# Kernel tuning notes

Hardware: AMD Instinct MI355X
Metric: run time of the kernel (lower is better)

The kernel has to match this reference:

```python
import jax, jax.numpy as jnp
import numpy as np

LAMBDA_K_TAU = 0.1
RIDGE = 0.1


def _masked_cov(x, mask, counts):
    """Covariance of masked rows. x: [B,S,D], mask: [B,S] float, counts: [B] float.
    Equivalent to packing the masked rows (batch_2d_tensor) then _torch_cov."""
    xm = x * mask[..., None]
    mean = xm.sum(axis=1) / counts[:, None]                 # [B,D]
    xc = (xm - mean[:, None, :]) * mask[..., None]          # [B,S,D]
    cov = jnp.einsum('bsi,bsj->bij', xc, xc)
    return cov / (counts - 1.0)[:, None, None]


def _calc_label_cov_inv(task_cov, label_cov):
    d = task_cov.shape[-1]
    eye = jnp.eye(d, dtype=task_cov.dtype)
    return jnp.linalg.inv(LAMBDA_K_TAU * label_cov + (1.0 - LAMBDA_K_TAU) * task_cov + RIDGE * eye)


def setup_inputs() -> dict:
    key = jax.random.key(0)
    ks = jax.random.split(key, 6)
    B, S, Q, D = 256, 512, 256, 512
    support_set = jax.random.normal(ks[0], (B, S, D), dtype=jnp.float32)
    support_labels = jax.random.randint(ks[1], (B, S), 0, 2, dtype=jnp.int32)
    query_set = jax.random.normal(ks[2], (B, Q, D), dtype=jnp.float32)
    # lengths in [len//2, len] so both classes are present and counts > 1
    support_set_lengths = jax.random.randint(ks[3], (B,), S // 2, S + 1, dtype=jnp.int32)
    query_set_lengths = jax.random.randint(ks[4], (B,), Q // 2, Q + 1, dtype=jnp.int32)
    log_prediction_scaling = jnp.asarray(np.log(10.0), dtype=jnp.float32)
    return {
        'support_set': support_set,
        'support_labels': support_labels,
        'query_set': query_set,
        'support_set_lengths': support_set_lengths,
        'query_set_lengths': query_set_lengths,
        'log_prediction_scaling': log_prediction_scaling,
    }


def reference(support_set, support_labels, query_set, support_set_lengths,
              query_set_lengths, log_prediction_scaling):
    B, S, D = support_set.shape
    Q = query_set.shape[1]
    f32 = support_set.dtype

    sup_valid = (jnp.arange(S)[None, :] < support_set_lengths[:, None]).astype(f32)  # [B,S]
    mask_pos = (support_labels == 1).astype(f32) * sup_valid                          # [B,S]
    mask_neg = (support_labels == 0).astype(f32) * sup_valid

    pos_counts = mask_pos.sum(axis=1)   # [B]
    neg_counts = mask_neg.sum(axis=1)
    sup_counts = support_set_lengths.astype(f32)

    positive_mean = jnp.einsum('bsd,bs->bd', support_set, mask_pos) / pos_counts[:, None]
    negative_mean = jnp.einsum('bsd,bs->bd', support_set, mask_neg) / neg_counts[:, None]

    cov_mats = _masked_cov(support_set, sup_valid, sup_counts)   # task covariance
    pos_mats = _masked_cov(support_set, mask_pos, pos_counts)    # == cov of packed positives
    neg_mats = _masked_cov(support_set, mask_neg, neg_counts)

    pos_inv = _calc_label_cov_inv(cov_mats, pos_mats)  # [B,D,D]
    neg_inv = _calc_label_cov_inv(cov_mats, neg_mats)

    q_valid = (jnp.arange(Q)[None, :] < query_set_lengths[:, None]).astype(f32)  # [B,Q]

    pos_diff = positive_mean[:, None, :] - query_set  # [B,Q,D]
    neg_diff = negative_mean[:, None, :] - query_set
    pos_maha = jnp.einsum('bik,bkx,bix->bi', pos_diff, pos_inv, pos_diff) * q_valid
    neg_maha = jnp.einsum('bik,bkx,bix->bi', neg_diff, neg_inv, neg_diff) * q_valid

    logit_scale = jnp.exp(log_prediction_scaling)
    # scale is applied inside batch_calculate_mahalanobis_logits AND again in forward
    logits = jnp.stack([neg_maha, pos_maha], axis=-1) * (-1.0) * logit_scale
    return logits * logit_scale  # [B,Q,2]
```

## Files before the change

kernel.cpp:

```cpp
#include <hip/hip_runtime.h>
#include <hip/hip_bf16.h>

#define TPB 256
constexpr int B_ = 256, S_ = 512, D_ = 512, Q_ = 256, NM_ = 512;
constexpr int NB = 64, NT = 8;

typedef _Float16 f16x8 __attribute__((ext_vector_type(8)));
typedef float f32x4 __attribute__((ext_vector_type(4)));

__device__ __forceinline__ void decode_mt(int bid, int W, int& m, int& t){
  int x = bid & 7, r = bid >> 3;
  t = r % W; int u = r / W;
  m = (((u >> 1)*8 + x) << 1) | (u & 1);
}

__device__ __forceinline__ void stage_D(const float* __restrict__ src, size_t ld,
                                        float (*dst)[68], int t)
{
  int r = t >> 2, seg = (t & 3) * 16;
  const float4* s4 = (const float4*)(src + (size_t)r*ld + seg);
  #pragma unroll
  for (int i=0;i<4;i++) *((float4*)&dst[r][seg + i*4]) = s4[i];
}

__device__ __forceinline__ void stage_T(const float* __restrict__ src, size_t ld,
                                        float (*dst)[68], int t)
{
  int r = t >> 2, seg = (t & 3) * 16;
  const float4* s4 = (const float4*)(src + (size_t)r*ld + seg);
  #pragma unroll
  for (int i=0;i<4;i++){
    float4 v = s4[i];
    dst[seg + i*4 + 0][r] = v.x;
    dst[seg + i*4 + 1][r] = v.y;
    dst[seg + i*4 + 2][r] = v.z;
    dst[seg + i*4 + 3][r] = v.w;
  }
}

__global__ __launch_bounds__(TPB) void k_stats(const float* __restrict__ X,
                                               const int* __restrict__ labels,
                                               const int* __restrict__ slen,
                                               float* __restrict__ mu,
                                               float* __restrict__ cnt,
                                               unsigned int* __restrict__ wpbits)
{
  int b = blockIdx.x, t = threadIdx.x;
  __shared__ int lab[S_];
  __shared__ float red[TPB];
  int L = slen[b];
  for (int s = t; s < S_; s += TPB) {
    int lb = labels[b*S_ + s];
    lab[s] = (s < L) ? lb : -1;
  }
  __syncthreads();
  if (t < 16) {
    unsigned int wword = 0;
    for (int i2 = 0; i2 < 32; i2++) if (lab[t*32 + i2] == 1) wword |= (1u << i2);
    wpbits[b*16 + t] = wword;
  }
  int cpi=0, cni=0;
  for (int s=t; s<S_; s+=TPB){ cpi += (lab[s]==1); cni += (lab[s]==0); }
  red[t] = (float)cpi; __syncthreads();
  for (int o=TPB/2;o>0;o>>=1){ if(t<o) red[t]+=red[t+o]; __syncthreads(); }
  float cp = red[0]; __syncthreads();
  red[t] = (float)cni; __syncthreads();
  for (int o=TPB/2;o>0;o>>=1){ if(t<o) red[t]+=red[t+o]; __syncthreads(); }
  float cn = red[0];
  if (t==0){ cnt[b*2+0]=cn; cnt[b*2+1]=cp; }
  float sp0=0,sp1=0,sn0=0,sn1=0;
  const float* Xb = X + (size_t)b*S_*D_;
  for (int s=0;s<S_;s++){
    int e = lab[s];
    if (e < 0) continue;
    float x0 = Xb[(size_t)s*D_ + t];
    float x1 = Xb[(size_t)s*D_ + t + 256];
    if (e==1){ sp0+=x0; sp1+=x1; } else { sn0+=x0; sn1+=x1; }
  }
  float stv = (float)L;
  float* mb = mu + (size_t)b*3*D_;
  mb[0*D_ + t] = sn0/cn;        mb[0*D_ + t+256] = sn1/cn;
  mb[1*D_ + t] = sp0/cp;        mb[1*D_ + t+256] = sp1/cp;
  mb[2*D_ + t] = (sn0+sp0)/stv; mb[2*D_ + t+256] = (sn1+sp1)/stv;
}

__global__ __launch_bounds__(TPB) void k_prep(const float* __restrict__ X,
                                              const int* __restrict__ slen,
                                              unsigned short* __restrict__ Xvh,
                                              unsigned short* __restrict__ Xvl)
{
  int b = blockIdx.y, z = blockIdx.x;
  int d0 = (z>>3)*64, s0 = (z&7)*64;
  int t = threadIdx.x;
  __shared__ float Tl[64][65];
  const float* src = X + ((size_t)b*S_ + s0)*D_ + d0;
  { int r = t>>2, seg = (t&3)*16;
    const float4* s4 = (const float4*)(src + (size_t)r*D_ + seg);
    #pragma unroll
    for (int i=0;i<4;i++){ float4 v = s4[i];
      Tl[seg+i*4+0][r]=v.x; Tl[seg+i*4+1][r]=v.y; Tl[seg+i*4+2][r]=v.z; Tl[seg+i*4+3][r]=v.w; } }
  __syncthreads();
  int L = slen[b];
  int dr = t>>2, sc = (t&3)*16;
  union U16 { unsigned short u[8]; uint4 v; };
  U16 H[2], Lo[2];
  #pragma unroll
  for (int g=0; g<2; g++)
    #pragma unroll
    for (int i=0;i<8;i++){
      int si = sc + g*8 + i;
      float x = (s0+si < L) ? Tl[dr][si] : 0.f;
      _Float16 hh = (_Float16)x;
      float lo = x - (float)hh;
      H[g].u[i]  = __builtin_bit_cast(unsigned short, hh);
      Lo[g].u[i] = __builtin_bit_cast(unsigned short, (_Float16)lo);
    }
  size_t o = ((size_t)b*D_ + d0+dr)*S_ + s0 + sc;
  *(uint4*)(Xvh+o)   = H[0].v;  *(uint4*)(Xvh+o+8) = H[1].v;
  *(uint4*)(Xvl+o)   = Lo[0].v; *(uint4*)(Xvl+o+8) = Lo[1].v;
}

__global__ __launch_bounds__(TPB,2) void k_gram(const unsigned short* __restrict__ Xvh,
                                                const unsigned short* __restrict__ Xvl,
                                                const unsigned int* __restrict__ wpbits,
                                                const float* __restrict__ mu,
                                                const float* __restrict__ cnt,
                                                const int* __restrict__ slen,
                                                float* __restrict__ A)
{
  __shared__ unsigned short sAvh[128][32], sAvl[128][32], sAph[128][32], sApl[128][32],
                            sBvh[128][32], sBvl[128][32];
  int id = blockIdx.x;
  int g = id>>3;
  int b = (g/10)*8 + (id&7);
  int z = g%10;
  int ti=0; while (z >= 4-ti){ z -= 4-ti; ti++; } int tj = ti + z;
  int i0 = ti*128, j0 = tj*128;
  int t = threadIdx.x, lane = t&63, w = t>>6;
  int wr = w>>1, wc = w&1, l15 = lane&15;

  f32x4 acc_t[4][4], acc_p[4][4];
  f32x4 z4 = {0.f,0.f,0.f,0.f};
  #pragma unroll
  for (int mf=0;mf<4;mf++)
    #pragma unroll
    for (int nf=0;nf<4;nf++){ acc_t[mf][nf]=z4; acc_p[mf][nf]=z4; }

  const size_t baseA = ((size_t)b*D_ + i0)*S_;
  const size_t baseB = ((size_t)b*D_ + j0)*S_;
  int phx = (lane>>4) ^ ((l15>>1)&3);

  for (int ks=0; ks<16; ks++){
    int s0 = ks*32;
    unsigned int wpw = wpbits[b*16 + ks];
    __syncthreads();
    #pragma unroll
    for (int h=0; h<2; h++){
      int ci = t + h*256;
      int row = ci>>2, cpos = ci&3;
      int ph = cpos ^ ((row>>1)&3);
      size_t ga = baseA + (size_t)row*S_ + s0 + cpos*8;
      size_t gb = baseB + (size_t)row*S_ + s0 + cpos*8;
      uint4 vh = *(const uint4*)(Xvh+ga);
      uint4 vl = *(const uint4*)(Xvl+ga);
      uint4 bh = *(const uint4*)(Xvh+gb);
      uint4 bl = *(const uint4*)(Xvl+gb);
      unsigned int m8 = (wpw >> (cpos*8)) & 0xFFu;
      uint4 mk;
      mk.x = ((m8&1u)?0xFFFFu:0u)  | ((m8&2u)?0xFFFF0000u:0u);
      mk.y = ((m8&4u)?0xFFFFu:0u)  | ((m8&8u)?0xFFFF0000u:0u);
      mk.z = ((m8&16u)?0xFFFFu:0u) | ((m8&32u)?0xFFFF0000u:0u);
      mk.w = ((m8&64u)?0xFFFFu:0u) | ((m8&128u)?0xFFFF0000u:0u);
      uint4 p4, q4;
      p4.x = vh.x&mk.x; p4.y = vh.y&mk.y; p4.z = vh.z&mk.z; p4.w = vh.w&mk.w;
      q4.x = vl.x&mk.x; q4.y = vl.y&mk.y; q4.z = vl.z&mk.z; q4.w = vl.w&mk.w;
      *(uint4*)&sAvh[row][ph*8] = vh;
      *(uint4*)&sAvl[row][ph*8] = vl;
      *(uint4*)&sAph[row][ph*8] = p4;
      *(uint4*)&sApl[row][ph*8] = q4;
      *(uint4*)&sBvh[row][ph*8] = bh;
      *(uint4*)&sBvl[row][ph*8] = bl;
    }
    __syncthreads();
    f16x8 Avh[4], Avl[4], Aph[4], Apl[4];
    #pragma unroll
    for (int mf=0;mf<4;mf++){
      int r = wr*64 + mf*16 + l15;
      Avh[mf] = __builtin_bit_cast(f16x8, *(const uint4*)&sAvh[r][phx*8]);
      Avl[mf] = __builtin_bit_cast(f16x8, *(const uint4*)&sAvl[r][phx*8]);
      Aph[mf] = __builtin_bit_cast(f16x8, *(const uint4*)&sAph[r][phx*8]);
      Apl[mf] = __builtin_bit_cast(f16x8, *(const uint4*)&sApl[r][phx*8]);
    }
    #pragma unroll
    for (int nf=0;nf<4;nf++){
      int r = wc*64 + nf*16 + l15;
      f16x8 Bh = __builtin_bit_cast(f16x8, *(const uint4*)&sBvh[r][phx*8]);
      f16x8 Bl = __builtin_bit_cast(f16x8, *(const uint4*)&sBvl[r][phx*8]);
      #pragma unroll
      for (int mf=0;mf<4;mf++){
        acc_t[mf][nf] = __builtin_amdgcn_mfma_f32_16x16x32_f16(Avh[mf], Bh, acc_t[mf][nf],0,0,0);
        acc_t[mf][nf] = __builtin_amdgcn_mfma_f32_16x16x32_f16(Avh[mf], Bl, acc_t[mf][nf],0,0,0);
        acc_t[mf][nf] = __builtin_amdgcn_mfma_f32_16x16x32_f16(Avl[mf], Bh, acc_t[mf][nf],0,0,0);
        acc_p[mf][nf] = __builtin_amdgcn_mfma_f32_16x16x32_f16(Aph[mf], Bh, acc_p[mf][nf],0,0,0);
        acc_p[mf][nf] = __builtin_amdgcn_mfma_f32_16x16x32_f16(Aph[mf], Bl, acc_p[mf][nf],0,0,0);
        acc_p[mf][nf] = __builtin_amdgcn_mfma_f32_16x16x32_f16(Apl[mf], Bh, acc_p[mf][nf],0,0,0);
      }
    }
  }
  float cn = cnt[b*2+0], cp = cnt[b*2+1];
  float stv = (float)slen[b];
  float kn = 0.1f/(cn-1.f), kp = 0.1f/(cp-1.f), kt = 0.9f/(stv-1.f);
  float rn = 0.1f*cn/(cn-1.f), rp = 0.1f*cp/(cp-1.f), rt = 0.9f*stv/(stv-1.f);
  const float* mb = mu + (size_t)b*3*D_;
  float* A0 = A + (size_t)(b*2+0)*D_*D_;
  float* A1 = A + (size_t)(b*2+1)*D_*D_;
  int rbase = i0 + wr*64 + (lane>>4)*4;
  int cbase = j0 + wc*64 + l15;
  #pragma unroll
  for (int mf=0;mf<4;mf++){
    #pragma unroll
    for (int i=0;i<4;i++){
      int r = rbase + mf*16 + i;
      float mnr = mb[r], mpr = mb[D_+r], mtr = mb[2*D_+r];
      #pragma unroll
      for (int nf=0;nf<4;nf++){
        int c = cbase + nf*16;
        float mnc = mb[c], mpc = mb[D_+c], mtc = mb[2*D_+c];
        float gp = acc_p[mf][nf][i];
        float gt = acc_t[mf][nf][i];
        float gn = gt - gp;
        float diag = (r==c)?0.1f:0.f;
        A0[(size_t)r*D_ + c] = kn*gn + kt*gt - rn*mnr*mnc - rt*mtr*mtc + diag;
        A1[(size_t)r*D_ + c] = kp*gp + kt*gt - rp*mpr*mpc - rt*mtr*mtc + diag;
      }
    }
  }
}

__global__ __launch_bounds__(TPB) void k_diag(float* __restrict__ A,
                                              float* __restrict__ invDT, int j)
{
  int m, t0; decode_mt(blockIdx.x, 1, m, t0); (void)t0;
  int t = threadIdx.x;
  __shared__ float Ld[64][65];
  __shared__ float Iv[64][65];
  float* Ab = A + (size_t)m*D_*D_ + (size_t)(j*NB)*D_ + j*NB;
  for (int l=t; l<4096; l+=TPB){ int r=l>>6, c=l&63; Ld[r][c] = Ab[(size_t)r*D_ + c]; Iv[r][c] = 0.f; }
  __syncthreads();
  for (int k=0;k<64;k++){
    if (t==0) Ld[k][k] = sqrtf(Ld[k][k]);
    __syncthreads();
    if (t>k && t<64) Ld[t][k] /= Ld[k][k];
    __syncthreads();
    for (int l=t; l<4096; l+=TPB){
      int r=l>>6, c=l&63;
      if (r>k && c>k) Ld[r][c] = fmaf(-Ld[r][k], Ld[c][k], Ld[r][c]);
    }
    __syncthreads();
  }
  if (t < 64){
    int c = t;
    Iv[c][c] = 1.f/Ld[c][c];
    for (int r=c+1;r<64;r++){
      float s = 0.f;
      for (int k2=c;k2<r;k2++) s += Ld[r][k2]*Iv[k2][c];
      Iv[r][c] = -s/Ld[r][r];
    }
  }
  __syncthreads();
  float* Ib = invDT + ((size_t)m*8 + j)*4096;
  for (int l=t; l<4096; l+=TPB){ Ib[l] = Iv[l&63][l>>6]; }
}

__global__ __launch_bounds__(TPB) void k_panel(float* __restrict__ A,
                                               const float* __restrict__ invDT,
                                               int j, int W)
{
  int m, ti; decode_mt(blockIdx.x, W, m, ti);
  int ib = j + 1 + ti;
  int t = threadIdx.x, tr = t&15, tc = t>>4;
  __shared__ float Ta[64][68], Tb[64][68];
  float* U = A + (size_t)m*D_*D_ + (size_t)(j*NB)*D_ + ib*NB;
  stage_D(invDT + ((size_t)m*8 + j)*4096, 64, Ta, t);
  stage_D(U, D_, Tb, t);
  __syncthreads();
  float acc[4][4] = {};
  for (int kk=0; kk<64; kk++){
    float4 av = *((const float4*)&Ta[kk][tr*4]);
    float4 bv = *((const float4*)&Tb[kk][tc*4]);
    float a[4]={av.x,av.y,av.z,av.w}, bb2[4]={bv.x,bv.y,bv.z,bv.w};
    #pragma unroll
    for (int u=0;u<4;u++)
      #pragma unroll
      for (int v=0;v<4;v++) acc[u][v] = fmaf(a[u], bb2[v], acc[u][v]);
  }
  #pragma unroll
  for (int u=0;u<4;u++){
    float4 o = make_float4(acc[u][0],acc[u][1],acc[u][2],acc[u][3]);
    *((float4*)(U + (size_t)(tr*4+u)*D_ + tc*4)) = o;
  }
}

__global__ __launch_bounds__(TPB) void k_trail(float* __restrict__ A, int j, int W)
{
  int m, z; decode_mt(blockIdx.x, W, m, z);
  int T = NT - 1 - j;
  int p = 0; while (z >= T - p){ z -= T - p; p++; }
  int a2 = j + 1 + p, b2 = a2 + z;
  int t = threadIdx.x, tr = t&15, tc = t>>4;
  __shared__ float Ta[64][68], Tb[64][68];
  float* Am = A + (size_t)m*D_*D_;
  stage_D(Am + (size_t)(j*NB)*D_ + a2*NB, D_, Ta, t);
  stage_D(Am + (size_t)(j*NB)*D_ + b2*NB, D_, Tb, t);
  __syncthreads();
  float acc[4][4] = {};
  for (int kk=0;kk<64;kk++){
    float4 av = *((const float4*)&Ta[kk][tr*4]);
    float4 bv = *((const float4*)&Tb[kk][tc*4]);
    float a[4]={av.x,av.y,av.z,av.w}, bb2[4]={bv.x,bv.y,bv.z,bv.w};
    #pragma unroll
    for (int u=0;u<4;u++)
      #pragma unroll
      for (int v=0;v<4;v++) acc[u][v] = fmaf(a[u], bb2[v], acc[u][v]);
  }
  float* Cb = Am + (size_t)(a2*NB)*D_ + b2*NB;
  #pragma unroll
  for (int u=0;u<4;u++){
    float4* pC = (float4*)(Cb + (size_t)(tr*4+u)*D_ + tc*4);
    float4 o = *pC;
    o.x -= acc[u][0]; o.y -= acc[u][1]; o.z -= acc[u][2]; o.w -= acc[u][3];
    *pC = o;
  }
}

__global__ __launch_bounds__(TPB) void k_solvefin(const float* __restrict__ Qs,
                                                  const float* __restrict__ mu,
                                                  const float* __restrict__ A,
                                                  const float* __restrict__ invDT,
                                                  float* __restrict__ Z,
                                                  const int* __restrict__ qlen,
                                                  const float* __restrict__ lps,
                                                  float* __restrict__ out)
{
  int m, t0; decode_mt(blockIdx.x, 4, m, t0);
  int q0 = t0*NB;
  int b = m>>1, cls = m&1;
  int t = threadIdx.x, tr = t&15, tc = t>>4;
  __shared__ float Ta[64][68], Tb[64][68];
  const float* Am = A + (size_t)m*D_*D_;
  float* Zm = Z + (size_t)m*D_*Q_;
  const float* muv = mu + ((size_t)b*3 + cls)*D_;
  float cs[4] = {0.f,0.f,0.f,0.f};
  for (int j=0;j<NT;j++){
    stage_T(Qs + ((size_t)b*Q_ + q0)*D_ + j*NB, D_, Ta, t);
    __syncthreads();
    float acc[4][4];
    #pragma unroll
    for (int u=0;u<4;u++){
      float mrow = muv[j*NB + tr*4 + u];
      #pragma unroll
      for (int v=0;v<4;v++) acc[u][v] = mrow - Ta[tr*4+u][tc*4+v];
    }
    __syncthreads();
    for (int k=0;k<j;k++){
      stage_D(Am + (size_t)(k*NB)*D_ + j*NB, D_, Ta, t);
      { int r = t >> 2, seg = (t & 3)*16;
        const float4* s4 = (const float4*)(Zm + (size_t)(k*NB + r)*Q_ + q0 + seg);
        #pragma unroll
        for (int i=0;i<4;i++) *((float4*)&Tb[r][seg + i*4]) = s4[i];
      }
      __syncthreads();
      for (int kk=0;kk<64;kk++){
        float4 av = *((const float4*)&Ta[kk][tr*4]);
        float4 bv = *((const float4*)&Tb[kk][tc*4]);
        float a[4]={av.x,av.y,av.z,av.w}, bb2[4]={bv.x,bv.y,bv.z,bv.w};
        #pragma unroll
        for (int u=0;u<4;u++)
          #pragma unroll
          for (int v=0;v<4;v++) acc[u][v] = fmaf(-a[u], bb2[v], acc[u][v]);
      }
      __syncthreads();
    }
    #pragma unroll
    for (int u=0;u<4;u++)
      #pragma unroll
      for (int v=0;v<4;v++) Tb[tr*4+u][tc*4+v] = acc[u][v];
    stage_D(invDT + ((size_t)m*8 + j)*4096, 64, Ta, t);
    __syncthreads();
    float o4[4][4] = {};
    for (int kk=0;kk<64;kk++){
      float4 av = *((const float4*)&Ta[kk][tr*4]);
      float4 bv = *((const float4*)&Tb[kk][tc*4]);
      float a[4]={av.x,av.y,av.z,av.w}, bb2[4]={bv.x,bv.y,bv.z,bv.w};
      #pragma unroll
      for (int u=0;u<4;u++)
        #pragma unroll
        for (int v=0;v<4;v++) o4[u][v] = fmaf(a[u], bb2[v], o4[u][v]);
    }
    if (j < NT-1){
      #pragma unroll
      for (int u=0;u<4;u++){
        float4 o = make_float4(o4[u][0], o4[u][1], o4[u][2], o4[u][3]);
        *((float4*)(Zm + (size_t)(j*NB + tr*4+u)*Q_ + q0 + tc*4)) = o;
      }
    }
    #pragma unroll
    for (int u=0;u<4;u++)
      #pragma unroll
      for (int v=0;v<4;v++) cs[v] = fmaf(o4[u][v], o4[u][v], cs[v]);
    __syncthreads();
  }
  float* red = &Ta[0][0];
  #pragma unroll
  for (int v=0;v<4;v++) red[(tc*4+v)*16 + tr] = cs[v];
  __syncthreads();
  if (t < 64){
    float s = 0.f;
    #pragma unroll
    for (int i=0;i<16;i++) s += red[t*16 + i];
    int q = q0 + t;
    float valid = (q < qlen[b]) ? 1.f : 0.f;
    float s2 = expf(2.f*lps[0]);
    out[((size_t)b*Q_ + q)*2 + cls] = -s2*s*valid;
  }
}

extern "C" void kernel_launch(void* const* d_in, const int* in_sizes, int n_in,
                              void* d_out, int out_size, void* d_ws, size_t ws_size,
                              hipStream_t stream) {
  (void)in_sizes; (void)n_in; (void)out_size;
  const float* X   = (const float*)d_in[0];
  const int*   lab = (const int*)d_in[1];
  const float* Qs  = (const float*)d_in[2];
  const int*   sl  = (const int*)d_in[3];
  const int*   ql  = (const int*)d_in[4];
  const float* lps = (const float*)d_in[5];
  float* out = (float*)d_out;

  float* A  = (float*)d_ws;
  float* Z  = A + (size_t)NM_*D_*D_;
  unsigned short* Xvh = (unsigned short*)Z;
  unsigned short* Xvl = Xvh + (size_t)B_*D_*S_;
  float* invDT = Z + (size_t)NM_*D_*Q_;
  float* mu   = invDT + (size_t)NM_*8*64*64;
  float* cnt  = mu + (size_t)B_*3*D_;
  unsigned int* wpbits = (unsigned int*)(cnt + B_*2);
  size_t need = (size_t)((char*)(wpbits + B_*16) - (char*)d_ws);
  if (ws_size < need) return;

  k_stats<<<dim3(B_), dim3(TPB), 0, stream>>>(X, lab, sl, mu, cnt, wpbits);
  k_prep<<<dim3(64, B_), dim3(TPB), 0, stream>>>(X, sl, Xvh, Xvl);
  k_gram<<<dim3(2560), dim3(TPB), 0, stream>>>(Xvh, Xvl, wpbits, mu, cnt, sl, A);
  for (int j=0; j<NT; j++){
    k_diag<<<dim3(NM_), dim3(TPB), 0, stream>>>(A, invDT, j);
    int nb = NT-1-j;
    if (nb > 0) k_panel<<<dim3(NM_*nb), dim3(TPB), 0, stream>>>(A, invDT, j, nb);
    int np = nb*(nb+1)/2;
    if (np > 0) k_trail<<<dim3(NM_*np), dim3(TPB), 0, stream>>>(A, j, np);
  }
  k_solvefin<<<dim3(NM_*4), dim3(TPB), 0, stream>>>(Qs, mu, A, invDT, Z, ql, lps, out);
}
```

Measured before the change: 2.743 ms.

## Fuse blocked Cholesky steps into one cooperative persistent kernel with grid syncs

The per-step diag, panel and trailing-update launches are replaced by one cooperative persistent kernel that walks all eight block steps, separated by grid-wide barriers. The next diagonal block's factorization and triangular inverse are folded into the trailing-update phase, so there is no separate serial diag launch per step. The triangular inverse is also parallelised across threads using shuffle reductions instead of one thread per column. The aim is to remove about twenty launches and the underused diag kernels. The cost is grid-sync overhead and possibly lower occupancy with 1024 resident blocks; if the cooperative launch fails, the old multi-kernel path is used.

```diff
diff --git a/kernel.cpp b/kernel.cpp
--- a/kernel.cpp
+++ b/kernel.cpp
@@ -1,5 +1,8 @@
 #include <hip/hip_runtime.h>
 #include <hip/hip_bf16.h>
+#include <hip/hip_cooperative_groups.h>
+
+namespace cg = cooperative_groups;
 
 #define TPB 256
 constexpr int B_ = 256, S_ = 512, D_ = 512, Q_ = 256, NM_ = 512;
@@ -13,6 +16,9 @@
   t = r % W; int u = r / W;
   m = (((u >> 1)*8 + x) << 1) | (u & 1);
 }
+__device__ __forceinline__ int mkm(int xcd, int u){
+  return (((u >> 1)*8 + xcd) << 1) | (u & 1);
+}
 
 __device__ __forceinline__ void stage_D(const float* __restrict__ src, size_t ld,
                                         float (*dst)[68], int t)
@@ -21,6 +27,14 @@
   const float4* s4 = (const float4*)(src + (size_t)r*ld + seg);
   #pragma unroll
   for (int i=0;i<4;i++) *((float4*)&dst[r][seg + i*4]) = s4[i];
+}
+__device__ __forceinline__ void stage68c(const float* __restrict__ src, size_t ld,
+                                         float* __restrict__ dst, int t)
+{
+  int r = t >> 2, seg = (t & 3) * 16;
+  const float4* s4 = (const float4*)(src + (size_t)r*ld + seg);
+  #pragma unroll
+  for (int i=0;i<4;i++) *((float4*)&dst[r*68 + seg + i*4]) = s4[i];
 }
 
 __device__ __forceinline__ void stage_T(const float* __restrict__ src, size_t ld,
@@ -237,6 +251,178 @@
   }
 }
 
+
+__device__ __forceinline__ void body_trail(const float* __restrict__ Pa,
+                                           const float* __restrict__ Pb,
+                                           float* __restrict__ Cb,
+                                           float* Ta, float* Tb, int t)
+{
+  int tr = t&15, tc = t>>4;
+  stage68c(Pa, D_, Ta, t);
+  stage68c(Pb, D_, Tb, t);
+  __syncthreads();
+  float acc[4][4] = {};
+  for (int kk=0;kk<64;kk++){
+    float4 av = *((const float4*)&Ta[kk*68 + tr*4]);
+    float4 bv = *((const float4*)&Tb[kk*68 + tc*4]);
+    float a[4]={av.x,av.y,av.z,av.w}, bb2[4]={bv.x,bv.y,bv.z,bv.w};
+    #pragma unroll
+    for (int u=0;u<4;u++)
+      #pragma unroll
+      for (int v=0;v<4;v++) acc[u][v] = fmaf(a[u], bb2[v], acc[u][v]);
+  }
+  #pragma unroll
+  for (int u=0;u<4;u++){
+    float4* pC = (float4*)(Cb + (size_t)(tr*4+u)*D_ + tc*4);
+    float4 o = *pC;
+    o.x -= acc[u][0]; o.y -= acc[u][1]; o.z -= acc[u][2]; o.w -= acc[u][3];
+    *pC = o;
+  }
+  __syncthreads();
+}
+
+__device__ __forceinline__ void body_panel(float* __restrict__ U,
+                                           const float* __restrict__ IDT,
+                                           float* Ta, float* Tb, int t)
+{
+  int tr = t&15, tc = t>>4;
+  stage68c(IDT, 64, Ta, t);
+  stage68c(U, D_, Tb, t);
+  __syncthreads();
+  float acc[4][4] = {};
+  for (int kk=0;kk<64;kk++){
+    float4 av = *((const float4*)&Ta[kk*68 + tr*4]);
+    float4 bv = *((const float4*)&Tb[kk*68 + tc*4]);
+    float a[4]={av.x,av.y,av.z,av.w}, bb2[4]={bv.x,bv.y,bv.z,bv.w};
+    #pragma unroll
+    for (int u=0;u<4;u++)
+      #pragma unroll
+      for (int v=0;v<4;v++) acc[u][v] = fmaf(a[u], bb2[v], acc[u][v]);
+  }
+  __syncthreads();
+  #pragma unroll
+  for (int u=0;u<4;u++){
+    float4 o = make_float4(acc[u][0],acc[u][1],acc[u][2],acc[u][3]);
+    *((float4*)(U + (size_t)(tr*4+u)*D_ + tc*4)) = o;
+  }
+  __syncthreads();
+}
+
+__device__ __forceinline__ void body_traildiag(const float* __restrict__ Pd,
+                                               const float* __restrict__ Cd,
+                                               float* __restrict__ Ig,
+                                               float* Ta, float* Tb, int t, bool dosub)
+{
+  int tr = t&15, tc = t>>4;
+  float acc[4][4] = {};
+  if (dosub){
+    stage68c(Pd, D_, Ta, t);
+    __syncthreads();
+    for (int kk=0;kk<64;kk++){
+      float4 av = *((const float4*)&Ta[kk*68 + tr*4]);
+      float4 bv = *((const float4*)&Ta[kk*68 + tc*4]);
+      float a[4]={av.x,av.y,av.z,av.w}, bb2[4]={bv.x,bv.y,bv.z,bv.w};
+      #pragma unroll
+      for (int u=0;u<4;u++)
+        #pragma unroll
+        for (int v=0;v<4;v++) acc[u][v] = fmaf(a[u], bb2[v], acc[u][v]);
+    }
+    __syncthreads();
+  }
+  float* Ld = Ta;
+  #pragma unroll
+  for (int u=0;u<4;u++){
+    float4 cv = *((const float4*)&Cd[(size_t)(tr*4+u)*D_ + tc*4]);
+    cv.x -= acc[u][0]; cv.y -= acc[u][1]; cv.z -= acc[u][2]; cv.w -= acc[u][3];
+    *((float4*)&Ld[(tr*4+u)*68 + tc*4]) = cv;
+  }
+  __syncthreads();
+  for (int k=0;k<64;k++){
+    if (t==0) Ld[k*68+k] = sqrtf(Ld[k*68+k]);
+    __syncthreads();
+    if (t>k && t<64) Ld[t*68+k] /= Ld[k*68+k];
+    __syncthreads();
+    for (int l=t; l<4096; l+=TPB){
+      int r=l>>6, c=l&63;
+      if (r>k && c>k) Ld[r*68+c] = fmaf(-Ld[r*68+k], Ld[c*68+k], Ld[r*68+c]);
+    }
+    __syncthreads();
+  }
+  {
+    int c = t>>2, s = t&3;
+    float myv[16];
+    #pragma unroll
+    for (int i=0;i<16;i++) myv[i] = 0.f;
+    if (s==0) myv[0] = 1.f/Ld[c*68+c];
+    for (int r=c+1;r<64;r++){
+      float partial = 0.f;
+      #pragma unroll
+      for (int idx=0; idx<16; idx++){
+        int k2 = c + s + 4*idx;
+        if (k2 < r) partial = fmaf(Ld[r*68+k2], myv[idx], partial);
+      }
+      partial += __shfl_xor(partial, 1, 64);
+      partial += __shfl_xor(partial, 2, 64);
+      float val = -partial / Ld[r*68+r];
+      int d = r - c;
+      #pragma unroll
+      for (int idx=0; idx<16; idx++)
+        if ((d & 3) == s && (d >> 2) == idx) myv[idx] = val;
+    }
+    #pragma unroll
+    for (int idx=0; idx<16; idx++){
+      int k2 = c + s + 4*idx;
+      if (k2 < 64) Ig[c*64 + k2] = myv[idx];
+    }
+  }
+  __syncthreads();
+}
+
+__global__ __launch_bounds__(256,4) void k_chol_coop(float* __restrict__ A,
+                                                     float* __restrict__ invDT)
+{
+  cg::grid_group grid = cg::this_grid();
+  __shared__ float sm[2*64*68];
+  float* Ta = sm; float* Tb = sm + 64*68;
+  int bid = blockIdx.x, t = threadIdx.x;
+  int xcd = bid & 7, lb = bid >> 3;
+  for (int lt=lb; lt<64; lt+=128){
+    int m = mkm(xcd, lt);
+    float* Am = A + (size_t)m*D_*D_;
+    body_traildiag(nullptr, Am, invDT + ((size_t)m*8 + 0)*4096, Ta, Tb, t, false);
+  }
+  grid.sync();
+  for (int j=0;j<7;j++){
+    int nbp = 7-j;
+    for (int lt=lb; lt<64*nbp; lt+=128){
+      int ti = lt>>6, ml = lt&63;
+      int m = mkm(xcd, ml); int ib = j+1+ti;
+      float* Am = A + (size_t)m*D_*D_;
+      body_panel(Am + (size_t)(j*NB)*D_ + ib*NB,
+                 invDT + ((size_t)m*8 + j)*4096, Ta, Tb, t);
+    }
+    grid.sync();
+    int np = nbp*(nbp+1)/2;
+    for (int lt=lb; lt<64*np; lt+=128){
+      int z = lt>>6, ml = lt&63;
+      int m = mkm(xcd, ml);
+      float* Am = A + (size_t)m*D_*D_;
+      int p=0, zz=z; while (zz >= nbp-p){ zz -= nbp-p; p++; }
+      int a = j+1+p, b = a+zz;
+      if (z == 0){
+        body_traildiag(Am + (size_t)(j*NB)*D_ + a*NB,
+                       Am + (size_t)(a*NB)*D_ + a*NB,
+                       invDT + ((size_t)m*8 + a)*4096, Ta, Tb, t, true);
+      } else {
+        body_trail(Am + (size_t)(j*NB)*D_ + a*NB,
+                   Am + (size_t)(j*NB)*D_ + b*NB,
+                   Am + (size_t)(a*NB)*D_ + b*NB, Ta, Tb, t);
+      }
+    }
+    grid.sync();
+  }
+}
+
 __global__ __launch_bounds__(TPB) void k_diag(float* __restrict__ A,
                                               float* __restrict__ invDT, int j)
 {
@@ -278,27 +464,10 @@
 {
   int m, ti; decode_mt(blockIdx.x, W, m, ti);
   int ib = j + 1 + ti;
-  int t = threadIdx.x, tr = t&15, tc = t>>4;
+  int t = threadIdx.x;
   __shared__ float Ta[64][68], Tb[64][68];
   float* U = A + (size_t)m*D_*D_ + (size_t)(j*NB)*D_ + ib*NB;
-  stage_D(invDT + ((size_t)m*8 + j)*4096, 64, Ta, t);
-  stage_D(U, D_, Tb, t);
-  __syncthreads();
-  float acc[4][4] = {};
-  for (int kk=0; kk<64; kk++){
-    float4 av = *((const float4*)&Ta[kk][tr*4]);
-    float4 bv = *((const float4*)&Tb[kk][tc*4]);
-    float a[4]={av.x,av.y,av.z,av.w}, bb2[4]={bv.x,bv.y,bv.z,bv.w};
-    #pragma unroll
-    for (int u=0;u<4;u++)
-      #pragma unroll
-      for (int v=0;v<4;v++) acc[u][v] = fmaf(a[u], bb2[v], acc[u][v]);
-  }
-  #pragma unroll
-  for (int u=0;u<4;u++){
-    float4 o = make_float4(acc[u][0],acc[u][1],acc[u][2],acc[u][3]);
-    *((float4*)(U + (size_t)(tr*4+u)*D_ + tc*4)) = o;
-  }
+  body_panel(U, invDT + ((size_t)m*8 + j)*4096, &Ta[0][0], &Tb[0][0], t);
 }
 
 __global__ __launch_bounds__(TPB) void k_trail(float* __restrict__ A, int j, int W)
@@ -307,30 +476,12 @@
   int T = NT - 1 - j;
   int p = 0; while (z >= T - p){ z -= T - p; p++; }
   int a2 = j + 1 + p, b2 = a2 + z;
-  int t = threadIdx.x, tr = t&15, tc = t>>4;
+  int t = threadIdx.x;
   __shared__ float Ta[64][68], Tb[64][68];
   float* Am = A + (size_t)m*D_*D_;
-  stage_D(Am + (size_t)(j*NB)*D_ + a2*NB, D_, Ta, t);
-  stage_D(Am + (size_t)(j*NB)*D_ + b2*NB, D_, Tb, t);
-  __syncthreads();
-  float acc[4][4] = {};
-  for (int kk=0;kk<64;kk++){
-    float4 av = *((const float4*)&Ta[kk][tr*4]);
-    float4 bv = *((const float4*)&Tb[kk][tc*4]);
-    float a[4]={av.x,av.y,av.z,av.w}, bb2[4]={bv.x,bv.y,bv.z,bv.w};
-    #pragma unroll
-    for (int u=0;u<4;u++)
-      #pragma unroll
-      for (int v=0;v<4;v++) acc[u][v] = fmaf(a[u], bb2[v], acc[u][v]);
-  }
-  float* Cb = Am + (size_t)(a2*NB)*D_ + b2*NB;
-  #pragma unroll
-  for (int u=0;u<4;u++){
-    float4* pC = (float4*)(Cb + (size_t)(tr*4+u)*D_ + tc*4);
-    float4 o = *pC;
-    o.x -= acc[u][0]; o.y -= acc[u][1]; o.z -= acc[u][2]; o.w -= acc[u][3];
-    *pC = o;
-  }
+  body_trail(Am + (size_t)(j*NB)*D_ + a2*NB,
+             Am + (size_t)(j*NB)*D_ + b2*NB,
+             Am + (size_t)(a2*NB)*D_ + b2*NB, &Ta[0][0], &Tb[0][0], t);
 }
 
 __global__ __launch_bounds__(TPB) void k_solvefin(const float* __restrict__ Qs,
@@ -451,12 +602,21 @@
   k_stats<<<dim3(B_), dim3(TPB), 0, stream>>>(X, lab, sl, mu, cnt, wpbits);
   k_prep<<<dim3(64, B_), dim3(TPB), 0, stream>>>(X, sl, Xvh, Xvl);
   k_gram<<<dim3(2560), dim3(TPB), 0, stream>>>(Xvh, Xvl, wpbits, mu, cnt, sl, A);
-  for (int j=0; j<NT; j++){
-    k_diag<<<dim3(NM_), dim3(TPB), 0, stream>>>(A, invDT, j);
-    int nb = NT-1-j;
-    if (nb > 0) k_panel<<<dim3(NM_*nb), dim3(TPB), 0, stream>>>(A, invDT, j, nb);
-    int np = nb*(nb+1)/2;
-    if (np > 0) k_trail<<<dim3(NM_*np), dim3(TPB), 0, stream>>>(A, j, np);
-  }
+
+  float* Aarg = A; float* Iarg = invDT;
+  void* cargs[] = { (void*)&Aarg, (void*)&Iarg };
+  hipError_t ce = hipLaunchCooperativeKernel((const void*)k_chol_coop,
+                                             dim3(1024), dim3(256), cargs, 0, stream);
+  if (ce != hipSuccess){
+    (void)hipGetLastError();
+    for (int j=0; j<NT; j++){
+      k_diag<<<dim3(NM_), dim3(TPB), 0, stream>>>(A, invDT, j);
+      int nb = NT-1-j;
+      if (nb > 0) k_panel<<<dim3(NM_*nb), dim3(TPB), 0, stream>>>(A, invDT, j, nb);
+      int np = nb*(nb+1)/2;
+      if (np > 0) k_trail<<<dim3(NM_*np), dim3(TPB), 0, stream>>>(A, j, np);
+    }
+  }
+
   k_solvefin<<<dim3(NM_*4), dim3(TPB), 0, stream>>>(Qs, mu, A, invDT, Z, ql, lps, out);
 }
```

Result: slower. 4.349 ms (+58.6%).

## Fuse blocked Cholesky diag, panel and trailing update into one step kernel

Applied to the files above, without the earlier changes.

Restructures the blocked Cholesky so each of the 7 steps is one launch: trailing blocks compute U^T-style updates via the stored diagonal inverse (W = Linv^T Linv), panel blocks write L below the diagonal, and the block owning the next diagonal tile also factors it and inverts it. This cuts kernel launches from 22 to 8 and removes the separate serialized diag kernel per step. It also parallelizes the triangular inversion across 4 lanes per column with shuffles. In exchange the trailing blocks do two 64x64 matmuls instead of one, and the diagonal block's serial Cholesky sits on the critical path inside a wide launch. The solve kernel is changed to read the lower-triangular layout.

```diff
diff --git a/kernel.cpp b/kernel.cpp
--- a/kernel.cpp
+++ b/kernel.cpp
@@ -21,6 +21,14 @@
   const float4* s4 = (const float4*)(src + (size_t)r*ld + seg);
   #pragma unroll
   for (int i=0;i<4;i++) *((float4*)&dst[r][seg + i*4]) = s4[i];
+}
+__device__ __forceinline__ void stage68c(const float* __restrict__ src, size_t ld,
+                                         float* __restrict__ dst, int t)
+{
+  int r = t >> 2, seg = (t & 3) * 16;
+  const float4* s4 = (const float4*)(src + (size_t)r*ld + seg);
+  #pragma unroll
+  for (int i=0;i<4;i++) *((float4*)&dst[r*68 + seg + i*4]) = s4[i];
 }
 
 __device__ __forceinline__ void stage_T(const float* __restrict__ src, size_t ld,
@@ -35,6 +43,21 @@
     dst[seg + i*4 + 1][r] = v.y;
     dst[seg + i*4 + 2][r] = v.z;
     dst[seg + i*4 + 3][r] = v.w;
+  }
+}
+
+__device__ __forceinline__ void mm_acc(const float* __restrict__ Aop,
+                                       const float* __restrict__ Bop,
+                                       float acc[4][4], int tr, int tc)
+{
+  for (int kk=0;kk<64;kk++){
+    float4 av = *((const float4*)&Aop[kk*68 + tr*4]);
+    float4 bv = *((const float4*)&Bop[kk*68 + tc*4]);
+    float a[4]={av.x,av.y,av.z,av.w}, b2[4]={bv.x,bv.y,bv.z,bv.w};
+    #pragma unroll
+    for (int u=0;u<4;u++)
+      #pragma unroll
+      for (int v=0;v<4;v++) acc[u][v] = fmaf(a[u], b2[v], acc[u][v]);
   }
 }
 
@@ -237,98 +260,154 @@
   }
 }
 
-__global__ __launch_bounds__(TPB) void k_diag(float* __restrict__ A,
-                                              float* __restrict__ invDT, int j)
-{
-  int m, t0; decode_mt(blockIdx.x, 1, m, t0); (void)t0;
-  int t = threadIdx.x;
-  __shared__ float Ld[64][65];
-  __shared__ float Iv[64][65];
-  float* Ab = A + (size_t)m*D_*D_ + (size_t)(j*NB)*D_ + j*NB;
-  for (int l=t; l<4096; l+=TPB){ int r=l>>6, c=l&63; Ld[r][c] = Ab[(size_t)r*D_ + c]; Iv[r][c] = 0.f; }
-  __syncthreads();
+__device__ __forceinline__ void diag_finish(float* __restrict__ Cd,
+                                            float* __restrict__ Ig,
+                                            float* Ld, float* Tb, int t)
+{
   for (int k=0;k<64;k++){
-    if (t==0) Ld[k][k] = sqrtf(Ld[k][k]);
-    __syncthreads();
-    if (t>k && t<64) Ld[t][k] /= Ld[k][k];
+    if (t==0) Ld[k*68+k] = sqrtf(Ld[k*68+k]);
+    __syncthreads();
+    if (t>k && t<64) Ld[t*68+k] /= Ld[k*68+k];
     __syncthreads();
     for (int l=t; l<4096; l+=TPB){
       int r=l>>6, c=l&63;
-      if (r>k && c>k) Ld[r][c] = fmaf(-Ld[r][k], Ld[c][k], Ld[r][c]);
-    }
-    __syncthreads();
-  }
-  if (t < 64){
-    int c = t;
-    Iv[c][c] = 1.f/Ld[c][c];
-    for (int r=c+1;r<64;r++){
-      float s = 0.f;
-      for (int k2=c;k2<r;k2++) s += Ld[r][k2]*Iv[k2][c];
-      Iv[r][c] = -s/Ld[r][r];
-    }
-  }
-  __syncthreads();
-  float* Ib = invDT + ((size_t)m*8 + j)*4096;
-  for (int l=t; l<4096; l+=TPB){ Ib[l] = Iv[l&63][l>>6]; }
-}
-
-__global__ __launch_bounds__(TPB) void k_panel(float* __restrict__ A,
-                                               const float* __restrict__ invDT,
-                                               int j, int W)
-{
-  int m, ti; decode_mt(blockIdx.x, W, m, ti);
-  int ib = j + 1 + ti;
+      if (r>k && c>k) Ld[r*68+c] = fmaf(-Ld[r*68+k], Ld[c*68+k], Ld[r*68+c]);
+    }
+    __syncthreads();
+  }
+  int c = t>>2, s = t&3;
+  float myv[16];
+  #pragma unroll
+  for (int i=0;i<16;i++) myv[i] = 0.f;
+  if (s==0) myv[0] = 1.f/Ld[c*68+c];
+  for (int r=c+1;r<64;r++){
+    float partial = 0.f;
+    #pragma unroll
+    for (int idx=0; idx<16; idx++){
+      int k2 = c + s + 4*idx;
+      if (k2 < r) partial = fmaf(Ld[r*68+k2], myv[idx], partial);
+    }
+    partial += __shfl_xor(partial, 1, 64);
+    partial += __shfl_xor(partial, 2, 64);
+    float val = -partial / Ld[r*68+r];
+    int d = r - c;
+    #pragma unroll
+    for (int idx=0; idx<16; idx++)
+      if ((d & 3) == s && (d >> 2) == idx) myv[idx] = val;
+  }
+  #pragma unroll
+  for (int idx=0; idx<16; idx++){
+    int k2 = c + s + 4*idx;
+    if (k2 < 64) Ig[c*64 + k2] = myv[idx];
+  }
+  for (int l=t; l<4352; l+=TPB) Tb[l] = 0.f;
+  __syncthreads();
+  #pragma unroll
+  for (int idx=0; idx<16; idx++){
+    int k2 = c + s + 4*idx;
+    if (k2 < 64) Tb[k2*68 + c] = myv[idx];
+  }
+  __syncthreads();
+  int tr = t&15, tc = t>>4;
+  float accW[4][4] = {};
+  mm_acc(Tb, Tb, accW, tr, tc);
+  #pragma unroll
+  for (int u=0;u<4;u++){
+    float4 o = make_float4(accW[u][0],accW[u][1],accW[u][2],accW[u][3]);
+    *((float4*)(Cd + (size_t)(tr*4+u)*D_ + tc*4)) = o;
+  }
+}
+
+__global__ __launch_bounds__(TPB) void k_diag0(float* __restrict__ A, float* __restrict__ invDT)
+{
+  int m, du; decode_mt(blockIdx.x, 1, m, du); (void)du;
+  int t = threadIdx.x;
+  __shared__ float Ta[64*68], Tb[64*68];
+  float* Am = A + (size_t)m*D_*D_;
+  stage68c(Am, D_, Ta, t);
+  __syncthreads();
+  diag_finish(Am, invDT + (size_t)m*8*4096, Ta, Tb, t);
+}
+
+__global__ __launch_bounds__(TPB) void k_step(float* __restrict__ A,
+                                              float* __restrict__ invDT,
+                                              int j, int np, int tot)
+{
+  __shared__ float Ta[64*68], Tb[64*68];
+  int m, z; decode_mt(blockIdx.x, tot, m, z);
   int t = threadIdx.x, tr = t&15, tc = t>>4;
-  __shared__ float Ta[64][68], Tb[64][68];
-  float* U = A + (size_t)m*D_*D_ + (size_t)(j*NB)*D_ + ib*NB;
-  stage_D(invDT + ((size_t)m*8 + j)*4096, 64, Ta, t);
-  stage_D(U, D_, Tb, t);
-  __syncthreads();
-  float acc[4][4] = {};
-  for (int kk=0; kk<64; kk++){
-    float4 av = *((const float4*)&Ta[kk][tr*4]);
-    float4 bv = *((const float4*)&Tb[kk][tc*4]);
-    float a[4]={av.x,av.y,av.z,av.w}, bb2[4]={bv.x,bv.y,bv.z,bv.w};
+  float* Am = A + (size_t)m*D_*D_;
+  const float* Wj = Am + (size_t)(j*NB)*D_ + j*NB;
+
+  if (z >= np){
+    int ti = j + 1 + (z - np);
+    stage68c(invDT + ((size_t)m*8 + j)*4096, 64, Ta, t);
+    stage68c(Am + (size_t)(j*NB)*D_ + ti*NB, D_, Tb, t);
+    __syncthreads();
+    float acc[4][4] = {};
+    mm_acc(Ta, Tb, acc, tr, tc);
+    float* Lout = Am + (size_t)(ti*NB)*D_ + j*NB;
+    #pragma unroll
+    for (int u=0;u<4;u++){
+      float4 o = make_float4(acc[u][0],acc[u][1],acc[u][2],acc[u][3]);
+      *((float4*)(Lout + (size_t)(tr*4+u)*D_ + tc*4)) = o;
+    }
+    return;
+  }
+
+  int Tn = NT - 1 - j;
+  int p = 0, zz = z;
+  while (zz >= Tn - p){ zz -= Tn - p; p++; }
+  int a = j + 1 + p, b = a + zz;
+
+  if (z == 0){
+    const float* Ud = Am + (size_t)(j*NB)*D_ + (j+1)*NB;
+    stage68c(Ud, D_, Ta, t);
+    stage68c(Wj, D_, Tb, t);
+    __syncthreads();
+    float accT[4][4] = {};
+    mm_acc(Tb, Ta, accT, tr, tc);
+    __syncthreads();
     #pragma unroll
     for (int u=0;u<4;u++)
       #pragma unroll
-      for (int v=0;v<4;v++) acc[u][v] = fmaf(a[u], bb2[v], acc[u][v]);
-  }
-  #pragma unroll
-  for (int u=0;u<4;u++){
-    float4 o = make_float4(acc[u][0],acc[u][1],acc[u][2],acc[u][3]);
-    *((float4*)(U + (size_t)(tr*4+u)*D_ + tc*4)) = o;
-  }
-}
-
-__global__ __launch_bounds__(TPB) void k_trail(float* __restrict__ A, int j, int W)
-{
-  int m, z; decode_mt(blockIdx.x, W, m, z);
-  int T = NT - 1 - j;
-  int p = 0; while (z >= T - p){ z -= T - p; p++; }
-  int a2 = j + 1 + p, b2 = a2 + z;
-  int t = threadIdx.x, tr = t&15, tc = t>>4;
-  __shared__ float Ta[64][68], Tb[64][68];
-  float* Am = A + (size_t)m*D_*D_;
-  stage_D(Am + (size_t)(j*NB)*D_ + a2*NB, D_, Ta, t);
-  stage_D(Am + (size_t)(j*NB)*D_ + b2*NB, D_, Tb, t);
-  __syncthreads();
-  float acc[4][4] = {};
-  for (int kk=0;kk<64;kk++){
-    float4 av = *((const float4*)&Ta[kk][tr*4]);
-    float4 bv = *((const float4*)&Tb[kk][tc*4]);
-    float a[4]={av.x,av.y,av.z,av.w}, bb2[4]={bv.x,bv.y,bv.z,bv.w};
-    #pragma unroll
-    for (int u=0;u<4;u++)
-      #pragma unroll
-      for (int v=0;v<4;v++) acc[u][v] = fmaf(a[u], bb2[v], acc[u][v]);
-  }
-  float* Cb = Am + (size_t)(a2*NB)*D_ + b2*NB;
+      for (int v=0;v<4;v++) Tb[(tr*4+u)*68 + tc*4+v] = accT[u][v];
+    __syncthreads();
+    float acc2[4][4] = {};
+    mm_acc(Ta, Tb, acc2, tr, tc);
+    __syncthreads();
+    float* Cd = Am + (size_t)((j+1)*NB)*D_ + (j+1)*NB;
+    #pragma unroll
+    for (int u=0;u<4;u++){
+      float4 cv = *((const float4*)(Cd + (size_t)(tr*4+u)*D_ + tc*4));
+      cv.x -= acc2[u][0]; cv.y -= acc2[u][1]; cv.z -= acc2[u][2]; cv.w -= acc2[u][3];
+      *((float4*)&Ta[(tr*4+u)*68 + tc*4]) = cv;
+    }
+    __syncthreads();
+    diag_finish(Cd, invDT + ((size_t)m*8 + j+1)*4096, Ta, Tb, t);
+    return;
+  }
+
+  stage68c(Am + (size_t)(j*NB)*D_ + b*NB, D_, Ta, t);
+  stage68c(Wj, D_, Tb, t);
+  __syncthreads();
+  float accT[4][4] = {};
+  mm_acc(Tb, Ta, accT, tr, tc);
+  __syncthreads();
+  #pragma unroll
+  for (int u=0;u<4;u++)
+    #pragma unroll
+    for (int v=0;v<4;v++) Tb[(tr*4+u)*68 + tc*4+v] = accT[u][v];
+  stage68c(Am + (size_t)(j*NB)*D_ + a*NB, D_, Ta, t);
+  __syncthreads();
+  float acc2[4][4] = {};
+  mm_acc(Ta, Tb, acc2, tr, tc);
+  float* Cb = Am + (size_t)(a*NB)*D_ + b*NB;
   #pragma unroll
   for (int u=0;u<4;u++){
     float4* pC = (float4*)(Cb + (size_t)(tr*4+u)*D_ + tc*4);
     float4 o = *pC;
-    o.x -= acc[u][0]; o.y -= acc[u][1]; o.z -= acc[u][2]; o.w -= acc[u][3];
+    o.x -= acc2[u][0]; o.y -= acc2[u][1]; o.z -= acc2[u][2]; o.w -= acc2[u][3];
     *pC = o;
   }
 }
@@ -363,7 +442,7 @@
     }
     __syncthreads();
     for (int k=0;k<j;k++){
-      stage_D(Am + (size_t)(k*NB)*D_ + j*NB, D_, Ta, t);
+      stage_D(Am + (size_t)(j*NB)*D_ + k*NB, D_, Ta, t);
       { int r = t >> 2, seg = (t & 3)*16;
         const float4* s4 = (const float4*)(Zm + (size_t)(k*NB + r)*Q_ + q0 + seg);
         #pragma unroll
@@ -451,12 +530,14 @@
   k_stats<<<dim3(B_), dim3(TPB), 0, stream>>>(X, lab, sl, mu, cnt, wpbits);
   k_prep<<<dim3(64, B_), dim3(TPB), 0, stream>>>(X, sl, Xvh, Xvl);
   k_gram<<<dim3(2560), dim3(TPB), 0, stream>>>(Xvh, Xvl, wpbits, mu, cnt, sl, A);
-  for (int j=0; j<NT; j++){
-    k_diag<<<dim3(NM_), dim3(TPB), 0, stream>>>(A, invDT, j);
-    int nb = NT-1-j;
-    if (nb > 0) k_panel<<<dim3(NM_*nb), dim3(TPB), 0, stream>>>(A, invDT, j, nb);
-    int np = nb*(nb+1)/2;
-    if (np > 0) k_trail<<<dim3(NM_*np), dim3(TPB), 0, stream>>>(A, j, np);
-  }
+
+  k_diag0<<<dim3(NM_), dim3(TPB), 0, stream>>>(A, invDT);
+  for (int j=0; j<7; j++){
+    int np = (7-j)*(8-j)/2;
+    int nb = 7-j;
+    int tot = np + nb;
+    k_step<<<dim3(NM_*tot), dim3(TPB), 0, stream>>>(A, invDT, j, np, tot);
+  }
+
   k_solvefin<<<dim3(NM_*4), dim3(TPB), 0, stream>>>(Qs, mu, A, invDT, Z, ql, lps, out);
 }
```

Measured after the change: 3.396 ms. +23.8%, slower.

## Fuse two trailing-update steps of blocked Cholesky and load query directly

Applied to the files above, without the earlier changes.

The blocked factorization now handles two panel columns per outer step. It updates only the next block row first, then applies a combined rank-128 trailing update in one kernel (k_trail2), so each trailing tile is read and written once per two panels instead of once per panel. Separately, the solve kernel drops its transposed shared-memory staging of the query tile and reads query rows straight from global memory as float4, removing two barriers per block column. The price is an extra small row-update launch per pair of steps, and the direct query loads are less coalesced.

```diff
diff --git a/kernel.cpp b/kernel.cpp
--- a/kernel.cpp
+++ b/kernel.cpp
@@ -23,18 +23,17 @@
   for (int i=0;i<4;i++) *((float4*)&dst[r][seg + i*4]) = s4[i];
 }
 
-__device__ __forceinline__ void stage_T(const float* __restrict__ src, size_t ld,
-                                        float (*dst)[68], int t)
-{
-  int r = t >> 2, seg = (t & 3) * 16;
-  const float4* s4 = (const float4*)(src + (size_t)r*ld + seg);
-  #pragma unroll
-  for (int i=0;i<4;i++){
-    float4 v = s4[i];
-    dst[seg + i*4 + 0][r] = v.x;
-    dst[seg + i*4 + 1][r] = v.y;
-    dst[seg + i*4 + 2][r] = v.z;
-    dst[seg + i*4 + 3][r] = v.w;
+__device__ __forceinline__ void mm_acc68(const float (*Aop)[68], const float (*Bop)[68],
+                                         float acc[4][4], int tr, int tc)
+{
+  for (int kk=0;kk<64;kk++){
+    float4 av = *((const float4*)&Aop[kk][tr*4]);
+    float4 bv = *((const float4*)&Bop[kk][tc*4]);
+    float a[4]={av.x,av.y,av.z,av.w}, b2[4]={bv.x,bv.y,bv.z,bv.w};
+    #pragma unroll
+    for (int u=0;u<4;u++)
+      #pragma unroll
+      for (int v=0;v<4;v++) acc[u][v] = fmaf(a[u], b2[v], acc[u][v]);
   }
 }
 
@@ -285,15 +284,7 @@
   stage_D(U, D_, Tb, t);
   __syncthreads();
   float acc[4][4] = {};
-  for (int kk=0; kk<64; kk++){
-    float4 av = *((const float4*)&Ta[kk][tr*4]);
-    float4 bv = *((const float4*)&Tb[kk][tc*4]);
-    float a[4]={av.x,av.y,av.z,av.w}, bb2[4]={bv.x,bv.y,bv.z,bv.w};
-    #pragma unroll
-    for (int u=0;u<4;u++)
-      #pragma unroll
-      for (int v=0;v<4;v++) acc[u][v] = fmaf(a[u], bb2[v], acc[u][v]);
-  }
+  mm_acc68(Ta, Tb, acc, tr, tc);
   #pragma unroll
   for (int u=0;u<4;u++){
     float4 o = make_float4(acc[u][0],acc[u][1],acc[u][2],acc[u][3]);
@@ -301,28 +292,49 @@
   }
 }
 
-__global__ __launch_bounds__(TPB) void k_trail(float* __restrict__ A, int j, int W)
+__global__ __launch_bounds__(TPB) void k_trailrow(float* __restrict__ A, int j, int row, int W)
 {
   int m, z; decode_mt(blockIdx.x, W, m, z);
-  int T = NT - 1 - j;
-  int p = 0; while (z >= T - p){ z -= T - p; p++; }
-  int a2 = j + 1 + p, b2 = a2 + z;
+  int b2 = row + z;
   int t = threadIdx.x, tr = t&15, tc = t>>4;
   __shared__ float Ta[64][68], Tb[64][68];
   float* Am = A + (size_t)m*D_*D_;
-  stage_D(Am + (size_t)(j*NB)*D_ + a2*NB, D_, Ta, t);
+  stage_D(Am + (size_t)(j*NB)*D_ + row*NB, D_, Ta, t);
   stage_D(Am + (size_t)(j*NB)*D_ + b2*NB, D_, Tb, t);
   __syncthreads();
   float acc[4][4] = {};
-  for (int kk=0;kk<64;kk++){
-    float4 av = *((const float4*)&Ta[kk][tr*4]);
-    float4 bv = *((const float4*)&Tb[kk][tc*4]);
-    float a[4]={av.x,av.y,av.z,av.w}, bb2[4]={bv.x,bv.y,bv.z,bv.w};
-    #pragma unroll
-    for (int u=0;u<4;u++)
-      #pragma unroll
-      for (int v=0;v<4;v++) acc[u][v] = fmaf(a[u], bb2[v], acc[u][v]);
-  }
+  mm_acc68(Ta, Tb, acc, tr, tc);
+  float* Cb = Am + (size_t)(row*NB)*D_ + b2*NB;
+  #pragma unroll
+  for (int u=0;u<4;u++){
+    float4* pC = (float4*)(Cb + (size_t)(tr*4+u)*D_ + tc*4);
+    float4 o = *pC;
+    o.x -= acc[u][0]; o.y -= acc[u][1]; o.z -= acc[u][2]; o.w -= acc[u][3];
+    *pC = o;
+  }
+}
+
+__global__ __launch_bounds__(TPB) void k_trail2(float* __restrict__ A, int jb, int W)
+{
+  int m, z; decode_mt(blockIdx.x, W, m, z);
+  int base = jb + 2;
+  int Tn = NT - base;
+  int p = 0, zz = z;
+  while (zz >= Tn - p){ zz -= Tn - p; p++; }
+  int a2 = base + p, b2 = a2 + zz;
+  int t = threadIdx.x, tr = t&15, tc = t>>4;
+  __shared__ float Ta[64][68], Tb[64][68];
+  float* Am = A + (size_t)m*D_*D_;
+  float acc[4][4] = {};
+  stage_D(Am + (size_t)(jb*NB)*D_ + a2*NB, D_, Ta, t);
+  stage_D(Am + (size_t)(jb*NB)*D_ + b2*NB, D_, Tb, t);
+  __syncthreads();
+  mm_acc68(Ta, Tb, acc, tr, tc);
+  __syncthreads();
+  stage_D(Am + (size_t)((jb+1)*NB)*D_ + a2*NB, D_, Ta, t);
+  stage_D(Am + (size_t)((jb+1)*NB)*D_ + b2*NB, D_, Tb, t);
+  __syncthreads();
+  mm_acc68(Ta, Tb, acc, tr, tc);
   float* Cb = Am + (size_t)(a2*NB)*D_ + b2*NB;
   #pragma unroll
   for (int u=0;u<4;u++){
@@ -352,16 +364,18 @@
   const float* muv = mu + ((size_t)b*3 + cls)*D_;
   float cs[4] = {0.f,0.f,0.f,0.f};
   for (int j=0;j<NT;j++){
-    stage_T(Qs + ((size_t)b*Q_ + q0)*D_ + j*NB, D_, Ta, t);
-    __syncthreads();
     float acc[4][4];
-    #pragma unroll
-    for (int u=0;u<4;u++){
-      float mrow = muv[j*NB + tr*4 + u];
-      #pragma unroll
-      for (int v=0;v<4;v++) acc[u][v] = mrow - Ta[tr*4+u][tc*4+v];
-    }
-    __syncthreads();
+    {
+      float4 mv = *(const float4*)&muv[j*NB + tr*4];
+      #pragma unroll
+      for (int v=0;v<4;v++){
+        float4 qv = *(const float4*)&Qs[((size_t)b*Q_ + q0 + tc*4 + v)*D_ + j*NB + tr*4];
+        acc[0][v] = mv.x - qv.x;
+        acc[1][v] = mv.y - qv.y;
+        acc[2][v] = mv.z - qv.z;
+        acc[3][v] = mv.w - qv.w;
+      }
+    }
     for (int k=0;k<j;k++){
       stage_D(Am + (size_t)(k*NB)*D_ + j*NB, D_, Ta, t);
       { int r = t >> 2, seg = (t & 3)*16;
@@ -451,12 +465,24 @@
   k_stats<<<dim3(B_), dim3(TPB), 0, stream>>>(X, lab, sl, mu, cnt, wpbits);
   k_prep<<<dim3(64, B_), dim3(TPB), 0, stream>>>(X, sl, Xvh, Xvl);
   k_gram<<<dim3(2560), dim3(TPB), 0, stream>>>(Xvh, Xvl, wpbits, mu, cnt, sl, A);
-  for (int j=0; j<NT; j++){
+
+  for (int j=0; j<NT; j+=2){
     k_diag<<<dim3(NM_), dim3(TPB), 0, stream>>>(A, invDT, j);
-    int nb = NT-1-j;
-    if (nb > 0) k_panel<<<dim3(NM_*nb), dim3(TPB), 0, stream>>>(A, invDT, j, nb);
-    int np = nb*(nb+1)/2;
-    if (np > 0) k_trail<<<dim3(NM_*np), dim3(TPB), 0, stream>>>(A, j, np);
-  }
+    int nb0 = NT-1-j;
+    if (nb0 > 0){
+      k_panel<<<dim3(NM_*nb0), dim3(TPB), 0, stream>>>(A, invDT, j, nb0);
+      int wr = NT - (j+1);
+      k_trailrow<<<dim3(NM_*wr), dim3(TPB), 0, stream>>>(A, j, j+1, wr);
+      k_diag<<<dim3(NM_), dim3(TPB), 0, stream>>>(A, invDT, j+1);
+      int nb1 = NT-1-(j+1);
+      if (nb1 > 0){
+        k_panel<<<dim3(NM_*nb1), dim3(TPB), 0, stream>>>(A, invDT, j+1, nb1);
+        int Tn = NT - (j+2);
+        int np = Tn*(Tn+1)/2;
+        if (np > 0) k_trail2<<<dim3(NM_*np), dim3(TPB), 0, stream>>>(A, j, np);
+      }
+    }
+  }
+
   k_solvefin<<<dim3(NM_*4), dim3(TPB), 0, stream>>>(Qs, mu, A, invDT, Z, ql, lps, out);
 }
```

Measured after the change: 2.657 ms. -3.1%, faster.
